# Performance work log

Measured on AMD Instinct MI355X. Metric: run time of the kernel, lower is better.

## Reference

```python
import jax, jax.numpy as jnp
import numpy as np

N = 170000      # nodes
E = 2400000     # edges
F_IN = 128      # dataset.num_features
H = 64          # hidden_channels
C = 40          # dataset.num_classes
L = 8           # num_layers
ENTROPY = 1.0   # args.entropy
EPS = 1e-20


def setup_inputs() -> dict:
    key = jax.random.key(0)
    ks = jax.random.split(key, 10)
    x = jax.random.normal(ks[0], (N, F_IN), jnp.float32)
    edge_src = jax.random.randint(ks[1], (E,), 0, N)
    edge_dst = jax.random.randint(ks[2], (E,), 0, N)
    edge_weight = jax.random.uniform(ks[3], (E,), jnp.float32) / 14.0  # ~1/deg scale
    u = jax.random.uniform(ks[4], (N, L + 1), jnp.float32, 1e-6, 1.0 - 1e-6)
    gumbel = -jnp.log(-jnp.log(u))  # standard Gumbel noise for gumbel_softmax
    lin0_w = jax.random.normal(ks[5], (F_IN, H), jnp.float32) / np.float32(np.sqrt(F_IN))
    lin0_b = jnp.zeros((H,), jnp.float32)
    meta_w = jax.random.normal(ks[6], (H, 1), jnp.float32) / np.float32(np.sqrt(H))
    meta_b = jnp.zeros((1,), jnp.float32)
    lin1_w = jax.random.normal(ks[7], (H, C), jnp.float32) / np.float32(np.sqrt(H))
    lin1_b = jnp.zeros((C,), jnp.float32)
    return dict(x=x, edge_weight=edge_weight, gumbel=gumbel,
                lin0_w=lin0_w, lin0_b=lin0_b, meta_w=meta_w, meta_b=meta_b,
                lin1_w=lin1_w, lin1_b=lin1_b,
                edge_src=edge_src, edge_dst=edge_dst)


def reference(x, edge_weight, gumbel, lin0_w, lin0_b, meta_w, meta_b,
              lin1_w, lin1_b, edge_src, edge_dst):
    # input projection + relu (dropout=0 -> no-op)
    x = jnp.maximum(x @ lin0_w + lin0_b, 0.0)  # [N,H]
    xs = [x]
    # GCNII layers with conv.alpha = conv.beta = 0 -> pure edge-weighted
    # scatter-add propagation followed by relu.
    for _ in range(L):
        msg = edge_weight[:, None] * x[edge_src]              # [E,H] gather
        x = jax.ops.segment_sum(msg, edge_dst, num_segments=N)  # [N,H] scatter-add
        x = jnp.maximum(x, 0.0)
        xs.append(x)
    xMat = jnp.stack(xs, axis=1)  # [N, L+1, H] (preds == xMatrix since concat='none')
    # MetaNet: [N, L+1]
    r = jnp.squeeze(xMat @ meta_w, -1) + meta_b[0]
    # get_t: stick-breaking with sigmoid; last column uses t=1 times cumprod
    s = jax.nn.sigmoid(r)                                    # [N, L+1]
    cp_excl = jnp.concatenate(
        [jnp.ones((N, 1), s.dtype), jnp.cumprod(1.0 - s, axis=1)[:, :-1]], axis=1)
    t = s * cp_excl
    t = t.at[:, -1].set(cp_excl[:, -1])
    ent_loss = ENTROPY * (-(jnp.log(t + EPS) * t).sum(1).mean())
    # gumbel_softmax(log(t+eps), tau=1, hard=False)
    tM = jax.nn.softmax(jnp.log(t + EPS) + gumbel, axis=1)   # [N, L+1]
    # layer mixing: [N,1,L+1] @ [N,L+1,H] -> [N,H]
    out = jnp.einsum('nl,nlh->nh', tM, xMat)
    out = out @ lin1_w + lin1_b
    return jax.nn.log_softmax(out, axis=-1), ent_loss
```

## Files before the change

### kernel.cpp

```cpp
#include <hip/hip_runtime.h>
#include <hip/hip_bf16.h>

#define N_NODES 170000
#define N_EDGES 2400000
#define F_IN_   128
#define H_      64
#define C_OUT   40
#define L_LAYERS 8
#define LP1     9
#define EPS_T   1e-20f
#define ROW_ELEMS (LP1 * H_)

typedef unsigned short u16;
typedef unsigned int u32;
typedef unsigned short u16x8 __attribute__((ext_vector_type(8)));
typedef short bf16x8 __attribute__((ext_vector_type(8)));
typedef float f32x4 __attribute__((ext_vector_type(4)));

__device__ __forceinline__ float bf2f(u16 u) {
    union { unsigned int i; float f; } c; c.i = ((unsigned int)u) << 16; return c.f;
}
__device__ __forceinline__ u16 f2bf(float f) {
    __hip_bfloat16 h = __float2bfloat16(f);
    return *reinterpret_cast<u16*>(&h);
}

__device__ __forceinline__ float waveReduceSum(float v) {
    for (int m = 32; m; m >>= 1) v += __shfl_xor(v, m, 64);
    return v;
}

__global__ __launch_bounds__(256) void k_zero4(float4* __restrict__ p) {
    p[blockIdx.x * 256 + threadIdx.x] = make_float4(0.f, 0.f, 0.f, 0.f);
}

__global__ __launch_bounds__(256) void k_hist(
    const int* __restrict__ edst, int* __restrict__ deg, int lo, int hi)
{
    int e = blockIdx.x * 256 + threadIdx.x;
    if (e >= N_EDGES) return;
    int d = edst[e];
    if (d < lo || d >= hi) return;
    atomicAdd(&deg[d], 1);
}

#define SCAN_TPB 256
#define SCAN_VPT 8
#define SCAN_EPB (SCAN_TPB * SCAN_VPT)
#define SCAN_BLOCKS ((N_NODES + SCAN_EPB - 1) / SCAN_EPB)

__global__ __launch_bounds__(SCAN_TPB) void k_scan1(
    const int* __restrict__ deg, int* __restrict__ rowstart,
    int* __restrict__ blockSums)
{
    __shared__ int tsum[SCAN_TPB];
    int tid = threadIdx.x;
    int base = blockIdx.x * SCAN_EPB + tid * SCAN_VPT;
    int vals[SCAN_VPT];
    int local = 0;
    #pragma unroll
    for (int i = 0; i < SCAN_VPT; ++i) {
        int idx = base + i;
        int v = (idx < N_NODES) ? deg[idx] : 0;
        vals[i] = local;
        local += v;
    }
    tsum[tid] = local;
    __syncthreads();
    for (int off = 1; off < SCAN_TPB; off <<= 1) {
        int v = (tid >= off) ? tsum[tid - off] : 0;
        __syncthreads();
        tsum[tid] += v;
        __syncthreads();
    }
    int texcl = tsum[tid] - local;
    #pragma unroll
    for (int i = 0; i < SCAN_VPT; ++i) {
        int idx = base + i;
        if (idx < N_NODES) rowstart[idx] = texcl + vals[i];
    }
    if (tid == SCAN_TPB - 1) blockSums[blockIdx.x] = tsum[tid];
}

__global__ __launch_bounds__(64) void k_scan2(int* __restrict__ blockSums) {
    if (threadIdx.x == 0) {
        int acc = 0;
        for (int i = 0; i < SCAN_BLOCKS; ++i) {
            int v = blockSums[i];
            blockSums[i] = acc;
            acc += v;
        }
    }
}

__global__ __launch_bounds__(SCAN_TPB) void k_scan3(
    int* __restrict__ rowstart, const int* __restrict__ blockSums)
{
    int off = blockSums[blockIdx.x];
    int base = blockIdx.x * SCAN_EPB + threadIdx.x * SCAN_VPT;
    #pragma unroll
    for (int i = 0; i < SCAN_VPT; ++i) {
        int idx = base + i;
        if (idx < N_NODES) rowstart[idx] += off;
    }
}

__global__ __launch_bounds__(256) void k_bucket(
    const int* __restrict__ esrc, const int* __restrict__ edst,
    const float* __restrict__ ew, const int* __restrict__ rowstart,
    int* __restrict__ cursor, int2* __restrict__ csr, int lo, int hi)
{
    int e = blockIdx.x * 256 + threadIdx.x;
    if (e >= N_EDGES) return;
    int d = edst[e];
    if (d < lo || d >= hi) return;
    int p = rowstart[d] + atomicAdd(&cursor[d], 1);
    csr[p] = make_int2(esrc[e], __float_as_int(ew[e]));
}

__global__ __launch_bounds__(256) void k_lin0(
    const float* __restrict__ x, const float* __restrict__ W0,
    const float* __restrict__ b0, u16* __restrict__ xMatB)
{
    __shared__ u16 Wt[H_ * F_IN_];
    int tid = threadIdx.x;
    for (int i = tid; i < F_IN_ * H_; i += 256) {
        int k = i >> 6, c = i & 63;
        Wt[c * F_IN_ + (k ^ ((c & 7) << 3))] = f2bf(W0[i]);
    }
    __syncthreads();

    int wave = tid >> 6, lane = tid & 63;
    int lg = lane >> 4;
    int lr = lane & 15;

    bf16x8 bfrag[4][4];
    float b0v[4];
    #pragma unroll
    for (int ct = 0; ct < 4; ++ct) {
        int c = ct * 16 + lr;
        #pragma unroll
        for (int kt = 0; kt < 4; ++kt) {
            int kidx = (kt * 32 + lg * 8) ^ ((c & 7) << 3);
            bfrag[ct][kt] = *reinterpret_cast<bf16x8*>(&Wt[c * F_IN_ + kidx]);
        }
        b0v[ct] = b0[c];
    }

    int nbase = blockIdx.x * 256 + wave * 64;
    #pragma unroll
    for (int m = 0; m < 4; ++m) {
        int arow = nbase + m * 16 + lr;
        int arowc = (arow < N_NODES) ? arow : (N_NODES - 1);
        const float4* xrow = (const float4*)(x + (size_t)arowc * F_IN_);
        f32x4 acc[4];
        #pragma unroll
        for (int ct = 0; ct < 4; ++ct) {
            acc[ct][0] = b0v[ct]; acc[ct][1] = b0v[ct];
            acc[ct][2] = b0v[ct]; acc[ct][3] = b0v[ct];
        }
        #pragma unroll
        for (int kt = 0; kt < 4; ++kt) {
            int k8 = kt * 8 + lg * 2;
            float4 xa = xrow[k8];
            float4 xb = xrow[k8 + 1];
            bf16x8 a;
            a[0] = (short)f2bf(xa.x); a[1] = (short)f2bf(xa.y);
            a[2] = (short)f2bf(xa.z); a[3] = (short)f2bf(xa.w);
            a[4] = (short)f2bf(xb.x); a[5] = (short)f2bf(xb.y);
            a[6] = (short)f2bf(xb.z); a[7] = (short)f2bf(xb.w);
            #pragma unroll
            for (int ct = 0; ct < 4; ++ct)
                acc[ct] = __builtin_amdgcn_mfma_f32_16x16x32_bf16(
                    a, bfrag[ct][kt], acc[ct], 0, 0, 0);
        }
        #pragma unroll
        for (int reg = 0; reg < 4; ++reg) {
            int n = nbase + m * 16 + lg * 4 + reg;
            if (n < N_NODES) {
                #pragma unroll
                for (int ct = 0; ct < 4; ++ct) {
                    float v = fmaxf(acc[ct][reg], 0.f);
                    xMatB[(size_t)n * ROW_ELEMS + ct * 16 + lr] = f2bf(v);
                }
            }
        }
    }
}

__global__ __launch_bounds__(256) void k_prop(
    const u16* __restrict__ xMatB, int l,
    const int* __restrict__ rowstart, const int* __restrict__ deg,
    const int2* __restrict__ csr, u16* __restrict__ xMatOut)
{
    int tid = threadIdx.x;
    int oc = tid & 7;
    int n = blockIdx.x * 32 + (tid >> 3);
    bool valid = (n < N_NODES);
    int start = valid ? rowstart[n] : 0;
    int d     = valid ? deg[n]      : 0;

    const unsigned loff = (unsigned)l * H_ + oc * 8;
    float acc0[8] = {0.f,0.f,0.f,0.f,0.f,0.f,0.f,0.f};
    float acc1[8] = {0.f,0.f,0.f,0.f,0.f,0.f,0.f,0.f};

    int t = 0;
    while (__any(t < d)) {
        if (t < d) {
            int2 e = csr[start + t];
            float w = __int_as_float(e.y);
            u16x8 v = *reinterpret_cast<const u16x8*>(
                &xMatB[(size_t)(unsigned)e.x * ROW_ELEMS + loff]);
            #pragma unroll
            for (int j = 0; j < 8; ++j) acc0[j] = fmaf(bf2f(v[j]), w, acc0[j]);
        }
        if (t + 1 < d) {
            int2 e = csr[start + t + 1];
            float w = __int_as_float(e.y);
            u16x8 v = *reinterpret_cast<const u16x8*>(
                &xMatB[(size_t)(unsigned)e.x * ROW_ELEMS + loff]);
            #pragma unroll
            for (int j = 0; j < 8; ++j) acc1[j] = fmaf(bf2f(v[j]), w, acc1[j]);
        }
        t += 2;
    }

    if (valid) {
        u16x8 o;
        #pragma unroll
        for (int j = 0; j < 8; ++j) o[j] = f2bf(fmaxf(acc0[j] + acc1[j], 0.f));
        __builtin_nontemporal_store(o, reinterpret_cast<u16x8*>(
            &xMatOut[(size_t)n * ROW_ELEMS + (l + 1) * H_ + oc * 8]));
    }
}

__global__ __launch_bounds__(256) void k_gatemix(
    const u16* __restrict__ xMatB, const float* __restrict__ gum,
    const float* __restrict__ mw, const float* __restrict__ mb,
    u16* __restrict__ mix, float* __restrict__ entPart)
{
    __shared__ float lds[4];
    int tid = threadIdx.x;
    int oc = tid & 7;
    int n = blockIdx.x * 32 + (tid >> 3);
    bool valid = (n < N_NODES);
    int nc = valid ? n : (N_NODES - 1);
    const u16* row = &xMatB[(size_t)nc * ROW_ELEMS + oc * 8];

    float mwv[8];
    #pragma unroll
    for (int q = 0; q < 8; ++q) mwv[q] = mw[oc * 8 + q];
    float mb0 = mb[0];

    u16x8 v[LP1];
    float r[LP1];
    #pragma unroll
    for (int j = 0; j < LP1; ++j) {
        v[j] = *reinterpret_cast<const u16x8*>(&row[j * H_]);
        float dot = 0.f;
        #pragma unroll
        for (int q = 0; q < 8; ++q) dot = fmaf(bf2f(v[j][q]), mwv[q], dot);
        dot += __shfl_xor(dot, 1, 64);
        dot += __shfl_xor(dot, 2, 64);
        dot += __shfl_xor(dot, 4, 64);
        r[j] = dot + mb0;
    }
    float gmine = valid ? gum[(size_t)n * LP1 + oc] : 0.f;
    float g8    = (valid && oc == 0) ? gum[(size_t)n * LP1 + 8] : 0.f;
    int gbase = tid & 56;

    float t[LP1], lg[LP1];
    float cp = 1.f;
    #pragma unroll
    for (int j = 0; j < LP1; ++j) {
        float s = 1.f / (1.f + expf(-r[j]));
        t[j] = (j == L_LAYERS) ? cp : s * cp;
        cp *= (1.f - s);
    }
    float ent = 0.f, mx = -INFINITY;
    #pragma unroll
    for (int j = 0; j < LP1; ++j) {
        float lt = logf(t[j] + EPS_T);
        ent -= t[j] * lt;
        float g = (j < 8) ? __shfl(gmine, (gbase & 56) + j, 64)
                          : __shfl(g8, gbase & 56, 64);
        lg[j] = lt + g;
        mx = fmaxf(mx, lg[j]);
    }
    float se = 0.f;
    #pragma unroll
    for (int j = 0; j < LP1; ++j) { lg[j] = expf(lg[j] - mx); se += lg[j]; }
    float inv = 1.f / se;

    float acc[8] = {0.f,0.f,0.f,0.f,0.f,0.f,0.f,0.f};
    #pragma unroll
    for (int j = 0; j < LP1; ++j) {
        float w = lg[j] * inv;
        #pragma unroll
        for (int q = 0; q < 8; ++q) acc[q] = fmaf(bf2f(v[j][q]), w, acc[q]);
    }
    if (valid) {
        u16x8 o;
        #pragma unroll
        for (int q = 0; q < 8; ++q) o[q] = f2bf(acc[q]);
        *reinterpret_cast<u16x8*>(&mix[(size_t)n * H_ + oc * 8]) = o;
    }

    float e = (valid && oc == 0) ? ent : 0.f;
    e = waveReduceSum(e);
    int wave = tid >> 6, lane = tid & 63;
    if (lane == 0) lds[wave] = e;
    __syncthreads();
    if (tid == 0) entPart[blockIdx.x] = lds[0] + lds[1] + lds[2] + lds[3];
}

__global__ __launch_bounds__(256) void k_lin1(
    const u16* __restrict__ mix, const float* __restrict__ W1,
    const float* __restrict__ b1, float* __restrict__ out)
{
    __shared__ u16 Wl[48 * 64];
    int tid = threadIdx.x;
    for (int i = tid; i < 48 * 64; i += 256) {
        int c = i >> 6, k = i & 63;
        float v = (c < C_OUT) ? W1[k * C_OUT + c] : 0.f;
        Wl[c * 64 + (k ^ ((c & 7) << 3))] = f2bf(v);
    }
    __syncthreads();

    int wave = tid >> 6, lane = tid & 63;
    int lg = lane >> 4, lr = lane & 15;

    bf16x8 bfrag[3][2];
    float b1v[3];
    #pragma unroll
    for (int ct = 0; ct < 3; ++ct) {
        int c = ct * 16 + lr;
        #pragma unroll
        for (int kt = 0; kt < 2; ++kt) {
            int kidx = (kt * 32 + lg * 8) ^ ((c & 7) << 3);
            bfrag[ct][kt] = *reinterpret_cast<bf16x8*>(&Wl[c * 64 + kidx]);
        }
        b1v[ct] = (c < C_OUT) ? b1[c] : 0.f;
    }

    int nbase = blockIdx.x * 64 + wave * 16;
    int arow = nbase + lr;
    int arowc = (arow < N_NODES) ? arow : (N_NODES - 1);
    const u16* mrow = &mix[(size_t)arowc * H_];

    f32x4 acc[3];
    #pragma unroll
    for (int ct = 0; ct < 3; ++ct) {
        acc[ct][0] = b1v[ct]; acc[ct][1] = b1v[ct];
        acc[ct][2] = b1v[ct]; acc[ct][3] = b1v[ct];
    }
    #pragma unroll
    for (int kt = 0; kt < 2; ++kt) {
        bf16x8 a = *reinterpret_cast<const bf16x8*>(&mrow[kt * 32 + lg * 8]);
        #pragma unroll
        for (int ct = 0; ct < 3; ++ct)
            acc[ct] = __builtin_amdgcn_mfma_f32_16x16x32_bf16(
                a, bfrag[ct][kt], acc[ct], 0, 0, 0);
    }
    #pragma unroll
    for (int reg = 0; reg < 4; ++reg) {
        float v0 = acc[0][reg], v1 = acc[1][reg];
        float v2 = (lr < 8) ? acc[2][reg] : -INFINITY;
        float mx = fmaxf(fmaxf(v0, v1), v2);
        mx = fmaxf(mx, __shfl_xor(mx, 1, 64));
        mx = fmaxf(mx, __shfl_xor(mx, 2, 64));
        mx = fmaxf(mx, __shfl_xor(mx, 4, 64));
        mx = fmaxf(mx, __shfl_xor(mx, 8, 64));
        float e = expf(v0 - mx) + expf(v1 - mx) + ((lr < 8) ? expf(v2 - mx) : 0.f);
        e += __shfl_xor(e, 1, 64);
        e += __shfl_xor(e, 2, 64);
        e += __shfl_xor(e, 4, 64);
        e += __shfl_xor(e, 8, 64);
        float ls = mx + logf(e);
        int n = nbase + lg * 4 + reg;
        if (n < N_NODES) {
            out[(size_t)n * C_OUT + lr]      = v0 - ls;
            out[(size_t)n * C_OUT + 16 + lr] = v1 - ls;
            if (lr < 8) out[(size_t)n * C_OUT + 32 + lr] = v2 - ls;
        }
    }
}

__global__ __launch_bounds__(256) void k_entreduce(
    const float* __restrict__ part, int n, float scale, float* __restrict__ out)
{
    __shared__ float lds[4];
    int tid = threadIdx.x;
    float s = 0.f;
    for (int i = tid; i < n; i += 256) s += part[i];
    s = waveReduceSum(s);
    int wave = tid >> 6, lane = tid & 63;
    if (lane == 0) lds[wave] = s;
    __syncthreads();
    if (tid == 0) out[0] = (lds[0] + lds[1] + lds[2] + lds[3]) * scale;
}

extern "C" void kernel_launch(void* const* d_in, const int* in_sizes, int n_in,
                              void* d_out, int out_size, void* d_ws, size_t ws_size,
                              hipStream_t stream)
{
    const float* x   = (const float*)d_in[0];
    const float* ew  = (const float*)d_in[1];
    const float* gum = (const float*)d_in[2];
    const float* W0  = (const float*)d_in[3];
    const float* b0  = (const float*)d_in[4];
    const float* mw  = (const float*)d_in[5];
    const float* mb  = (const float*)d_in[6];
    const float* W1  = (const float*)d_in[7];
    const float* b1  = (const float*)d_in[8];
    const int* esrc  = (const int*)d_in[9];
    const int* edst  = (const int*)d_in[10];
    float* out = (float*)d_out;

    const int propBlocks = (N_NODES + 31) / 32;

    const size_t xMatBytes = (size_t)N_NODES * ROW_ELEMS * sizeof(u16);
    const size_t degBytes  = (size_t)N_NODES * sizeof(int);
    const size_t curBytes  = (size_t)N_NODES * sizeof(int);
    const size_t rowBytes  = (size_t)N_NODES * sizeof(int);
    const size_t bsBytes   = 512;
    const size_t csrBytes  = (size_t)N_EDGES * sizeof(int2);
    const size_t mixBytes  = (size_t)N_NODES * H_ * sizeof(u16);
    const size_t entBytes  = (size_t)propBlocks * sizeof(float);
    const size_t need = xMatBytes + degBytes + curBytes + rowBytes + bsBytes +
                        csrBytes + mixBytes + entBytes;
    if (ws_size < need) return;

    char* p = (char*)d_ws;
    u16*  xMatB    = (u16*)p;           p += xMatBytes;
    int*  deg      = (int*)p;           p += degBytes;
    int*  cursor   = (int*)p;           p += curBytes;
    int*  rowstart = (int*)p;           p += rowBytes;
    int*  blockSums= (int*)p;           p += bsBytes;
    int2* csr      = (int2*)p;          p += csrBytes;
    u16*  mixbuf   = (u16*)p;           p += mixBytes;
    float* entP    = (float*)p;

    const int edgeBlocks = (N_EDGES + 255) / 256;
    const int lin0Blocks = (N_NODES + 255) / 256;
    const int gmixBlocks = propBlocks;
    const int lin1Blocks = (N_NODES + 63) / 64;

    k_zero4<<<333, 256, 0, stream>>>((float4*)deg);
    const int STEP_H = N_NODES / 4;
    for (int i = 0; i < 4; ++i)
        k_hist<<<edgeBlocks, 256, 0, stream>>>(edst, deg, i * STEP_H,
                                               (i + 1) * STEP_H);
    k_scan1<<<SCAN_BLOCKS, SCAN_TPB, 0, stream>>>(deg, rowstart, blockSums);
    k_scan2<<<1, 64, 0, stream>>>(blockSums);
    k_scan3<<<SCAN_BLOCKS, SCAN_TPB, 0, stream>>>(rowstart, blockSums);
    const int STEP_B = N_NODES / 8;
    for (int i = 0; i < 8; ++i)
        k_bucket<<<edgeBlocks, 256, 0, stream>>>(esrc, edst, ew, rowstart,
                                                 cursor, csr, i * STEP_B,
                                                 (i + 1) * STEP_B);

    k_lin0<<<lin0Blocks, 256, 0, stream>>>(x, W0, b0, xMatB);
    for (int l = 0; l < L_LAYERS; ++l)
        k_prop<<<propBlocks, 256, 0, stream>>>(xMatB, l, rowstart, deg, csr,
                                               xMatB);
    k_gatemix<<<gmixBlocks, 256, 0, stream>>>(xMatB, gum, mw, mb, mixbuf, entP);
    k_lin1<<<lin1Blocks, 256, 0, stream>>>(mixbuf, W1, b1, out);
    k_entreduce<<<1, 256, 0, stream>>>(entP, gmixBlocks, 1.0f / N_NODES,
                                       out + (size_t)N_NODES * C_OUT);
}
```

Baseline: 839.9 us.

## Sort nodes by degree so propagation waves process similar-degree rows

Adds a degree histogram, a scan and a scatter that build a degree-sorted node permutation with permuted rowstart and degree arrays. The propagation kernel then maps each 8-thread group to a permuted slot, so a wave handles nodes of similar degree. This is meant to cut the divergence where the __any loop runs to the largest degree in the wave. It costs three small extra kernels and extra arrays. It also adds an indirection, and the output writes of neighbouring groups now go to scattered nodes, which loses write locality.

Result: slower. 1.314 ms (+56.5%).

```diff
diff --git a/kernel.cpp b/kernel.cpp
--- a/kernel.cpp
+++ b/kernel.cpp
@@ -116,6 +116,46 @@
     if (d < lo || d >= hi) return;
     int p = rowstart[d] + atomicAdd(&cursor[d], 1);
     csr[p] = make_int2(esrc[e], __float_as_int(ew[e]));
+}
+
+__global__ __launch_bounds__(256) void k_degbin(
+    const int* __restrict__ deg, int* __restrict__ bins)
+{
+    __shared__ int h[64];
+    int tid = threadIdx.x;
+    if (tid < 64) h[tid] = 0;
+    __syncthreads();
+    for (int n = blockIdx.x * 256 + tid; n < N_NODES; n += gridDim.x * 256) {
+        int d = deg[n]; if (d > 63) d = 63;
+        atomicAdd(&h[d], 1);
+    }
+    __syncthreads();
+    if (tid < 64 && h[tid] > 0) atomicAdd(&bins[tid], h[tid]);
+}
+
+__global__ __launch_bounds__(64) void k_degscan(int* __restrict__ binsBuf) {
+    if (threadIdx.x == 0) {
+        int acc = 0;
+        for (int i = 0; i < 64; ++i) {
+            binsBuf[64 + i] = acc;
+            acc += binsBuf[i];
+        }
+    }
+}
+
+__global__ __launch_bounds__(256) void k_degscatter(
+    const int* __restrict__ deg, const int* __restrict__ rowstart,
+    int* __restrict__ binsBuf, int* __restrict__ perm,
+    int* __restrict__ rowstartP, int* __restrict__ degP)
+{
+    int n = blockIdx.x * 256 + threadIdx.x;
+    if (n >= N_NODES) return;
+    int d = deg[n];
+    int db = (d > 63) ? 63 : d;
+    int pos = binsBuf[64 + db] + atomicAdd(&binsBuf[128 + db], 1);
+    perm[pos] = n;
+    rowstartP[pos] = rowstart[n];
+    degP[pos] = d;
 }
 
 __global__ __launch_bounds__(256) void k_lin0(
@@ -190,15 +230,17 @@
 
 __global__ __launch_bounds__(256) void k_prop(
     const u16* __restrict__ xMatB, int l,
-    const int* __restrict__ rowstart, const int* __restrict__ deg,
+    const int* __restrict__ perm, const int* __restrict__ rowstartP,
+    const int* __restrict__ degP,
     const int2* __restrict__ csr, u16* __restrict__ xMatOut)
 {
     int tid = threadIdx.x;
     int oc = tid & 7;
-    int n = blockIdx.x * 32 + (tid >> 3);
-    bool valid = (n < N_NODES);
-    int start = valid ? rowstart[n] : 0;
-    int d     = valid ? deg[n]      : 0;
+    int slot = blockIdx.x * 32 + (tid >> 3);
+    bool valid = (slot < N_NODES);
+    int n     = valid ? perm[slot]      : 0;
+    int start = valid ? rowstartP[slot] : 0;
+    int d     = valid ? degP[slot]      : 0;
 
     const unsigned loff = (unsigned)l * H_ + oc * 8;
     float acc0[8] = {0.f,0.f,0.f,0.f,0.f,0.f,0.f,0.f};
@@ -427,8 +469,11 @@
     const size_t csrBytes  = (size_t)N_EDGES * sizeof(int2);
     const size_t mixBytes  = (size_t)N_NODES * H_ * sizeof(u16);
     const size_t entBytes  = (size_t)propBlocks * sizeof(float);
+    const size_t permBytes = (size_t)N_NODES * sizeof(int);
+    const size_t binsBytes = 4096;
     const size_t need = xMatBytes + degBytes + curBytes + rowBytes + bsBytes +
-                        csrBytes + mixBytes + entBytes;
+                        csrBytes + mixBytes + entBytes + 3 * permBytes +
+                        binsBytes;
     if (ws_size < need) return;
 
     char* p = (char*)d_ws;
@@ -439,14 +484,20 @@
     int*  blockSums= (int*)p;           p += bsBytes;
     int2* csr      = (int2*)p;          p += csrBytes;
     u16*  mixbuf   = (u16*)p;           p += mixBytes;
-    float* entP    = (float*)p;
+    float* entP    = (float*)p;         p += entBytes;
+    int*  perm     = (int*)p;           p += permBytes;
+    int*  rowstartP= (int*)p;           p += permBytes;
+    int*  degP     = (int*)p;           p += permBytes;
+    int*  binsBuf  = (int*)p;
 
     const int edgeBlocks = (N_EDGES + 255) / 256;
     const int lin0Blocks = (N_NODES + 255) / 256;
     const int gmixBlocks = propBlocks;
     const int lin1Blocks = (N_NODES + 63) / 64;
+    const int nodeBlocks = (N_NODES + 255) / 256;
 
     k_zero4<<<333, 256, 0, stream>>>((float4*)deg);
+    k_zero4<<<1, 256, 0, stream>>>((float4*)binsBuf);
     const int STEP_H = N_NODES / 4;
     for (int i = 0; i < 4; ++i)
         k_hist<<<edgeBlocks, 256, 0, stream>>>(edst, deg, i * STEP_H,
@@ -460,10 +511,15 @@
                                                  cursor, csr, i * STEP_B,
                                                  (i + 1) * STEP_B);
 
+    k_degbin<<<256, 256, 0, stream>>>(deg, binsBuf);
+    k_degscan<<<1, 64, 0, stream>>>(binsBuf);
+    k_degscatter<<<nodeBlocks, 256, 0, stream>>>(deg, rowstart, binsBuf,
+                                                 perm, rowstartP, degP);
+
     k_lin0<<<lin0Blocks, 256, 0, stream>>>(x, W0, b0, xMatB);
     for (int l = 0; l < L_LAYERS; ++l)
-        k_prop<<<propBlocks, 256, 0, stream>>>(xMatB, l, rowstart, deg, csr,
-                                               xMatB);
+        k_prop<<<propBlocks, 256, 0, stream>>>(xMatB, l, perm, rowstartP, degP,
+                                               csr, xMatB);
     k_gatemix<<<gmixBlocks, 256, 0, stream>>>(xMatB, gum, mw, mb, mixbuf, entP);
     k_lin1<<<lin1Blocks, 256, 0, stream>>>(mixbuf, W1, b1, out);
     k_entreduce<<<1, 256, 0, stream>>>(entP, gmixBlocks, 1.0f / N_NODES,
```
